# Kernel optimization log

Hardware: AMD Instinct MI355X
Metric: run time of the kernel (lower is better)

Reference implementation:

```python
import jax, jax.numpy as jnp
import numpy as np

B, C = 2048, 512          # batch, channels
CHG = 16                  # coarse grid side (16x16 -> N=256)
FHG = 16                  # fine grid side (16x16 -> F=256)
N = CHG * CHG             # coarse_span.total
F = FHG * FHG             # fine_total
K = 4                     # top4 sample mode
LOG_F = float(np.log(F))


def _ln(x, g, b, eps=1e-5):
    m = jnp.mean(x, axis=-1, keepdims=True)
    v = jnp.var(x, axis=-1, keepdims=True)
    return (x - m) * jax.lax.rsqrt(v + eps) * g + b


def _mlp3(x, w1, b1, w2, b2, w3, b3):
    # linear_stack: Linear+gelu, Linear+gelu, Linear (dropout=0 / eval)
    h = jax.nn.gelu(x @ w1 + b1)
    h = jax.nn.gelu(h @ w2 + b2)
    return h @ w3 + b3


def setup_inputs() -> dict:
    key = jax.random.key(0)
    ks = jax.random.split(key, 10)
    s = 0.02
    return {
        'x': jax.random.normal(ks[0], (B, C), jnp.float32),
        'in_g': jnp.ones((C,), jnp.float32), 'in_b': jnp.zeros((C,), jnp.float32),
        'nop_w': jax.random.normal(ks[1], (C, 1), jnp.float32) * s,
        'nop_b': jnp.zeros((1,), jnp.float32),
        'c_w1': jax.random.normal(ks[2], (C, C), jnp.float32) * s,
        'c_b1': jnp.zeros((C,), jnp.float32),
        'c_w2': jax.random.normal(ks[3], (C, C), jnp.float32) * s,
        'c_b2': jnp.zeros((C,), jnp.float32),
        'c_w3': jax.random.normal(ks[4], (C, N), jnp.float32) * s,
        'c_b3': jnp.zeros((N,), jnp.float32),
        'emb': jax.random.normal(ks[5], (N, C), jnp.float32),
        'emb_g': jnp.ones((C,), jnp.float32), 'emb_b': jnp.zeros((C,), jnp.float32),
        'f_w1': jax.random.normal(ks[6], (2 * C, C), jnp.float32) * s,
        'f_b1': jnp.zeros((C,), jnp.float32),
        'f_w2': jax.random.normal(ks[7], (C, C), jnp.float32) * s,
        'f_b2': jnp.zeros((C,), jnp.float32),
        'f_w3': jax.random.normal(ks[8], (C, F), jnp.float32) * s,
        'f_b3': jnp.zeros((F,), jnp.float32),
    }


def reference(x, in_g, in_b, nop_w, nop_b, c_w1, c_b1, c_w2, c_b2, c_w3, c_b3,
              emb, emb_g, emb_b, f_w1, f_b1, f_w2, f_b2, f_w3, f_b3):
    xn = _ln(x, in_g, in_b)                                  # (B,C)
    no_op = xn @ nop_w + nop_b                               # (B,1)
    coarse = _mlp3(xn, c_w1, c_b1, c_w2, c_b2, c_w3, c_b3)   # (B,N)
    _, idx = jax.lax.top_k(coarse, K)                        # (B,K) int32
    e = _ln(emb[idx], emb_g, emb_b)                          # (B,K,C)
    fin = jnp.concatenate([jnp.broadcast_to(xn[:, None, :], (B, K, C)), e], axis=-1)
    fine = _mlp3(fin, f_w1, f_b1, f_w2, f_b2, f_w3, f_b3)    # (B,K,F)
    # scatter value: coarse[b,i] - log F + fine + log F - lse(fine) = coarse[b,i] + log_softmax(fine)
    vals = jnp.take_along_axis(coarse, idx, axis=1)[:, :, None] + jax.nn.log_softmax(fine, axis=-1)
    dense = jnp.broadcast_to((coarse - LOG_F)[:, :, None], (B, N, F))
    dense = dense.at[jnp.arange(B)[:, None], idx].set(vals)  # top-k indices are distinct
    # view (B, ch0, ch1, fh0, fh1) -> permute (0,1,3,2,4) -> flatten
    xname = dense.reshape(B, CHG, CHG, FHG, FHG).transpose(0, 1, 3, 2, 4).reshape(B, -1)
    return jnp.concatenate([no_op, xname], axis=-1)          # (B, 1 + N*F)
```

## Files before the change

kernel.cpp:

```cpp
#include <hip/hip_runtime.h>
#include <math.h>

#define BATCH 2048
#define CH 512
#define N_COARSE 256
#define F_FINE 256
#define K_TOP 4
#define OUT_STRIDE 65537

typedef unsigned short ushort_t;
typedef __bf16 bf16x8 __attribute__((ext_vector_type(8)));
typedef float f32x4 __attribute__((ext_vector_type(4)));

__device__ __forceinline__ float gelu_tanh(float x) {
    float x3 = x * x * x;
    float t = tanhf(0.7978845608028654f * (x + 0.044715f * x3));
    return 0.5f * x * (1.0f + t);
}

__device__ __forceinline__ ushort_t f2bf(float f) {
    unsigned u = __float_as_uint(f);
    unsigned r = (u + 0x7FFF + ((u >> 16) & 1)) >> 16;
    return (ushort_t)r;
}

__global__ __launch_bounds__(256) void prep_kernel(
    const float* __restrict__ w1, const float* __restrict__ w2, const float* __restrict__ w3,
    ushort_t* __restrict__ t1, ushort_t* __restrict__ t2, ushort_t* __restrict__ t3,
    const float* __restrict__ x, const float* __restrict__ g, const float* __restrict__ b,
    const float* __restrict__ nop_w, const float* __restrict__ nop_b,
    float* __restrict__ xn, ushort_t* __restrict__ xn_bf, float* __restrict__ out)
{
    int blk = blockIdx.x;
    int t = threadIdx.x;
    if (blk < 896) {
        __shared__ float s[32][33];
        const float* W; ushort_t* Wt; int Kd, Nd, gx, gy;
        if (blk < 512)      { W = w1; Wt = t1; Kd = 1024; Nd = 512; gx = blk & 15; gy = blk >> 4; }
        else if (blk < 768) { W = w2; Wt = t2; Kd = 512;  Nd = 512; gx = (blk - 512) & 15; gy = (blk - 512) >> 4; }
        else                { W = w3; Wt = t3; Kd = 512;  Nd = 256; gx = (blk - 768) & 7;  gy = (blk - 768) >> 3; }
        int tx = t & 31, ty = t >> 5;
        int n0 = gx * 32, k0 = gy * 32;
        #pragma unroll
        for (int i = 0; i < 4; ++i) {
            int r = ty + i * 8;
            s[r][tx] = W[(size_t)(k0 + r) * Nd + n0 + tx];
        }
        __syncthreads();
        #pragma unroll
        for (int i = 0; i < 4; ++i) {
            int r = ty + i * 8;
            Wt[(size_t)(n0 + r) * Kd + k0 + tx] = f2bf(s[tx][r]);
        }
    } else {
        int row = blk - 896;
        int lane = t & 63, wave = t >> 6;
        const float* xr = x + (size_t)row * CH;
        float v0 = xr[t], v1 = xr[t + 256];
        float s = v0 + v1, ss = v0 * v0 + v1 * v1;
        #pragma unroll
        for (int off = 32; off; off >>= 1) { s += __shfl_xor(s, off); ss += __shfl_xor(ss, off); }
        __shared__ float red[8];
        if (lane == 0) { red[wave] = s; red[4 + wave] = ss; }
        __syncthreads();
        s = red[0] + red[1] + red[2] + red[3];
        ss = red[4] + red[5] + red[6] + red[7];
        float mean = s * (1.0f / CH);
        float var = ss * (1.0f / CH) - mean * mean;
        float rsq = rsqrtf(var + 1e-5f);
        float xn0 = (v0 - mean) * rsq * g[t] + b[t];
        float xn1 = (v1 - mean) * rsq * g[t + 256] + b[t + 256];
        float* xnr = xn + (size_t)row * CH;
        xnr[t] = xn0; xnr[t + 256] = xn1;
        ushort_t* xbr = xn_bf + (size_t)row * CH;
        xbr[t] = f2bf(xn0); xbr[t + 256] = f2bf(xn1);
        float d = xn0 * nop_w[t] + xn1 * nop_w[t + 256];
        #pragma unroll
        for (int off = 32; off; off >>= 1) d += __shfl_xor(d, off);
        __syncthreads();
        if (lane == 0) red[wave] = d;
        __syncthreads();
        if (t == 0) out[(size_t)row * OUT_STRIDE] = red[0] + red[1] + red[2] + red[3] + nop_b[0];
    }
}

template<bool GELU>
__global__ __launch_bounds__(256) void gemm_kernel(
    const float* __restrict__ A, const float* __restrict__ W,
    const float* __restrict__ bias, float* __restrict__ Cmat, int Nd, int Kd)
{
    __shared__ float As[2][32][68];
    __shared__ float Ws[2][32][36];
    int t = threadIdx.x;
    int tx = t & 7, ty = t >> 3;
    int n0 = blockIdx.x * 32, m0 = blockIdx.y * 64;

    float4 aR[2]; float4 wR;
    float acc[2][4] = {};

    auto loadAB = [&](int k0) {
        #pragma unroll
        for (int i = 0; i < 2; ++i) {
            int c = i * 256 + t;
            aR[i] = *(const float4*)&A[(size_t)(m0 + (c >> 3)) * Kd + k0 + (c & 7) * 4];
        }
        wR = *(const float4*)&W[(size_t)(k0 + (t >> 3)) * Nd + n0 + (t & 7) * 4];
    };
    auto storeAB = [&](int p) {
        #pragma unroll
        for (int i = 0; i < 2; ++i) {
            int c = i * 256 + t, r = c >> 3, kq = (c & 7) * 4;
            As[p][kq + 0][r] = aR[i].x; As[p][kq + 1][r] = aR[i].y;
            As[p][kq + 2][r] = aR[i].z; As[p][kq + 3][r] = aR[i].w;
        }
        *(float4*)&Ws[p][t >> 3][(t & 7) * 4] = wR;
    };

    loadAB(0);
    storeAB(0);
    int steps = Kd >> 5;
    int p = 0;
    for (int s = 0; s < steps; ++s) {
        __syncthreads();
        if (s + 1 < steps) loadAB((s + 1) * 32);
        #pragma unroll
        for (int kk = 0; kk < 32; ++kk) {
            float2 a = *(const float2*)&As[p][kk][ty * 2];
            float4 w = *(const float4*)&Ws[p][kk][tx * 4];
            acc[0][0] += a.x * w.x; acc[0][1] += a.x * w.y; acc[0][2] += a.x * w.z; acc[0][3] += a.x * w.w;
            acc[1][0] += a.y * w.x; acc[1][1] += a.y * w.y; acc[1][2] += a.y * w.z; acc[1][3] += a.y * w.w;
        }
        if (s + 1 < steps) storeAB(p ^ 1);
        p ^= 1;
    }

    #pragma unroll
    for (int i = 0; i < 2; ++i) {
        int gm = m0 + ty * 2 + i;
        int gn0 = n0 + tx * 4;
        float4 o;
        float* po = &o.x;
        #pragma unroll
        for (int j = 0; j < 4; ++j) {
            float v = acc[i][j] + bias[gn0 + j];
            if (GELU) v = gelu_tanh(v);
            po[j] = v;
        }
        *(float4*)&Cmat[(size_t)gm * Nd + gn0] = o;
    }
}

template<int MT, int NT, bool CONCAT, bool GELU, bool OUT_BF16, bool LOGSM>
__global__ __launch_bounds__(256) void mfma_gemm_kernel(
    const ushort_t* __restrict__ A1, const ushort_t* __restrict__ A2, int K1,
    const ushort_t* __restrict__ Wt, const float* __restrict__ bias,
    const float* __restrict__ cvals, void* __restrict__ Cout, int Nd, int Ktot)
{
    constexpr int AI = MT / 64, BI = NT / 64;
    constexpr int FI = MT / 32, FJ = NT / 32;
    __shared__ ushort_t As[2][MT * 32];
    __shared__ ushort_t Bs[2][NT * 32];
    __shared__ float mxs[64][2];
    __shared__ float ses[64][2];
    int t = threadIdx.x;
    int n0 = blockIdx.x * NT, m0 = blockIdx.y * MT;
    int wave = t >> 6, lane = t & 63;
    int wm = (wave & 1) * (MT / 2), wn = (wave >> 1) * (NT / 2);
    int lr = lane & 15, quad = lane >> 4;

    f32x4 acc[FI][FJ] = {};
    float4 aReg[AI], bReg[BI];

    auto loadAB = [&](int k0) {
        #pragma unroll
        for (int i = 0; i < AI; ++i) {
            int c = i * 256 + t, r = c >> 2, q = (c & 3) * 8;
            int gr = m0 + r;
            const ushort_t* ap;
            if (CONCAT) ap = (k0 < K1) ? A1 + (size_t)(gr >> 2) * K1 + k0 + q
                                       : A2 + (size_t)gr * (Ktot - K1) + (k0 - K1) + q;
            else        ap = A1 + (size_t)gr * Ktot + k0 + q;
            aReg[i] = *(const float4*)ap;
        }
        #pragma unroll
        for (int i = 0; i < BI; ++i) {
            int c = i * 256 + t, r = c >> 2, q = (c & 3) * 8;
            bReg[i] = *(const float4*)(Wt + (size_t)(n0 + r) * Ktot + k0 + q);
        }
    };
    auto storeAB = [&](int p) {
        #pragma unroll
        for (int i = 0; i < AI; ++i) { int c = i * 256 + t; *(float4*)&As[p][c * 8] = aReg[i]; }
        #pragma unroll
        for (int i = 0; i < BI; ++i) { int c = i * 256 + t; *(float4*)&Bs[p][c * 8] = bReg[i]; }
    };

    loadAB(0);
    storeAB(0);
    int steps = Ktot >> 5;
    int p = 0;
    for (int s = 0; s < steps; ++s) {
        __syncthreads();
        if (s + 1 < steps) loadAB((s + 1) * 32);
        bf16x8 af[FI], bfr[FJ];
        #pragma unroll
        for (int i = 0; i < FI; ++i)
            af[i] = *(const bf16x8*)&As[p][(wm + i * 16 + lr) * 32 + quad * 8];
        #pragma unroll
        for (int j = 0; j < FJ; ++j)
            bfr[j] = *(const bf16x8*)&Bs[p][(wn + j * 16 + lr) * 32 + quad * 8];
        #pragma unroll
        for (int i = 0; i < FI; ++i)
            #pragma unroll
            for (int j = 0; j < FJ; ++j)
                acc[i][j] = __builtin_amdgcn_mfma_f32_16x16x32_bf16(af[i], bfr[j], acc[i][j], 0, 0, 0);
        if (s + 1 < steps) storeAB(p ^ 1);
        p ^= 1;
    }

    if (LOGSM) {
        float bv[FJ];
        #pragma unroll
        for (int j = 0; j < FJ; ++j) bv[j] = bias[wn + j * 16 + lr];
        int half = wave >> 1;
        float rmx[FI][4];
        #pragma unroll
        for (int i = 0; i < FI; ++i)
            #pragma unroll
            for (int r = 0; r < 4; ++r) {
                float m = -1e30f;
                #pragma unroll
                for (int j = 0; j < FJ; ++j) m = fmaxf(m, acc[i][j][r] + bv[j]);
                #pragma unroll
                for (int mk = 1; mk < 16; mk <<= 1) m = fmaxf(m, __shfl_xor(m, mk));
                if (lr == 0) mxs[wm + i * 16 + quad * 4 + r][half] = m;
            }
        __syncthreads();
        #pragma unroll
        for (int i = 0; i < FI; ++i)
            #pragma unroll
            for (int r = 0; r < 4; ++r) {
                int rl = wm + i * 16 + quad * 4 + r;
                rmx[i][r] = fmaxf(mxs[rl][0], mxs[rl][1]);
            }
        #pragma unroll
        for (int i = 0; i < FI; ++i)
            #pragma unroll
            for (int r = 0; r < 4; ++r) {
                float s = 0.f;
                #pragma unroll
                for (int j = 0; j < FJ; ++j) s += expf(acc[i][j][r] + bv[j] - rmx[i][r]);
                #pragma unroll
                for (int mk = 1; mk < 16; mk <<= 1) s += __shfl_xor(s, mk);
                if (lr == 0) ses[wm + i * 16 + quad * 4 + r][half] = s;
            }
        __syncthreads();
        float* outp = (float*)Cout;
        #pragma unroll
        for (int i = 0; i < FI; ++i)
            #pragma unroll
            for (int r = 0; r < 4; ++r) {
                int rl = wm + i * 16 + quad * 4 + r;
                float se = ses[rl][0] + ses[rl][1];
                float addc = cvals[m0 + rl] - rmx[i][r] - logf(se);
                #pragma unroll
                for (int j = 0; j < FJ; ++j)
                    outp[(size_t)(m0 + rl) * Nd + wn + j * 16 + lr] = acc[i][j][r] + bv[j] + addc;
            }
    } else {
        #pragma unroll
        for (int j = 0; j < FJ; ++j) {
            int col = n0 + wn + j * 16 + lr;
            float bvv = bias[col];
            #pragma unroll
            for (int i = 0; i < FI; ++i) {
                #pragma unroll
                for (int r = 0; r < 4; ++r) {
                    int row = m0 + wm + i * 16 + quad * 4 + r;
                    float val = acc[i][j][r] + bvv;
                    if (GELU) val = gelu_tanh(val);
                    if (OUT_BF16)
                        ((ushort_t*)Cout)[(size_t)row * Nd + col] = f2bf(val);
                    else
                        ((float*)Cout)[(size_t)row * Nd + col] = val;
                }
            }
        }
    }
}

__global__ __launch_bounds__(256) void topk_embln_kernel(
    const float* __restrict__ coarse, const float* __restrict__ emb,
    const float* __restrict__ g, const float* __restrict__ b,
    int* __restrict__ idx, float* __restrict__ cvals, ushort_t* __restrict__ e_bf)
{
    int brow = blockIdx.x;
    int t = threadIdx.x;
    int wave = t >> 6, lane = t & 63;
    __shared__ int sidx[4];

    if (wave == 0) {
        const float* cr = coarse + (size_t)brow * N_COARSE;
        float v[4]; int id[4];
        #pragma unroll
        for (int j = 0; j < 4; ++j) { v[j] = cr[lane + 64 * j]; id[j] = lane + 64 * j; }
        #pragma unroll
        for (int r = 0; r < K_TOP; ++r) {
            float bv = v[0]; int bi = id[0];
            #pragma unroll
            for (int j = 1; j < 4; ++j)
                if (v[j] > bv || (v[j] == bv && id[j] < bi)) { bv = v[j]; bi = id[j]; }
            #pragma unroll
            for (int off = 32; off; off >>= 1) {
                float ov = __shfl_xor(bv, off); int oi = __shfl_xor(bi, off);
                if (ov > bv || (ov == bv && oi < bi)) { bv = ov; bi = oi; }
            }
            if ((bi & 63) == lane) v[bi >> 6] = -INFINITY;
            if (lane == 0) {
                sidx[r] = bi;
                idx[brow * K_TOP + r] = bi;
                cvals[brow * K_TOP + r] = bv;
            }
        }
    }
    __syncthreads();

    int n = sidx[wave];
    const float* er = emb + (size_t)n * CH + lane * 8;
    float4 u0 = *(const float4*)er;
    float4 u1 = *(const float4*)(er + 4);
    float s  = u0.x + u0.y + u0.z + u0.w + u1.x + u1.y + u1.z + u1.w;
    float ss = u0.x * u0.x + u0.y * u0.y + u0.z * u0.z + u0.w * u0.w
             + u1.x * u1.x + u1.y * u1.y + u1.z * u1.z + u1.w * u1.w;
    #pragma unroll
    for (int off = 32; off; off >>= 1) { s += __shfl_xor(s, off); ss += __shfl_xor(ss, off); }
    float mean = s * (1.0f / CH);
    float var = ss * (1.0f / CH) - mean * mean;
    float rsq = rsqrtf(var + 1e-5f);
    float4 g0 = *(const float4*)(g + lane * 8), g1 = *(const float4*)(g + lane * 8 + 4);
    float4 b0 = *(const float4*)(b + lane * 8), b1 = *(const float4*)(b + lane * 8 + 4);
    uint4 pk;
    pk.x = (unsigned)f2bf((u0.x - mean) * rsq * g0.x + b0.x) |
           ((unsigned)f2bf((u0.y - mean) * rsq * g0.y + b0.y) << 16);
    pk.y = (unsigned)f2bf((u0.z - mean) * rsq * g0.z + b0.z) |
           ((unsigned)f2bf((u0.w - mean) * rsq * g0.w + b0.w) << 16);
    pk.z = (unsigned)f2bf((u1.x - mean) * rsq * g1.x + b1.x) |
           ((unsigned)f2bf((u1.y - mean) * rsq * g1.y + b1.y) << 16);
    pk.w = (unsigned)f2bf((u1.z - mean) * rsq * g1.z + b1.z) |
           ((unsigned)f2bf((u1.w - mean) * rsq * g1.w + b1.w) << 16);
    *(uint4*)(e_bf + (size_t)(brow * K_TOP + wave) * CH + lane * 8) = pk;
}

__global__ __launch_bounds__(256) void scatter_kernel(
    const float* __restrict__ coarse, const float* __restrict__ fine,
    const int* __restrict__ idx, float* __restrict__ out)
{
    const float LOG_F = 5.545177444479562f;
    int b = blockIdx.y;
    __shared__ int sidx[4];
    if (threadIdx.x < 4) sidx[threadIdx.x] = idx[b * 4 + threadIdx.x];
    __syncthreads();
    int i0 = sidx[0], i1 = sidx[1], i2 = sidx[2], i3 = sidx[3];
    size_t rowb = (size_t)b * OUT_STRIDE + 1;
    #pragma unroll
    for (int q = 0; q < 4; ++q) {
        int o = blockIdx.x * 4096 + q * 1024 + threadIdx.x * 4;
        int c0 = o >> 12, f0 = (o >> 8) & 15, c1 = (o >> 4) & 15, f1 = o & 15;
        int n = c0 * 16 + c1;
        int f = f0 * 16 + f1;
        int k = -1;
        if (n == i0) k = 0; else if (n == i1) k = 1; else if (n == i2) k = 2; else if (n == i3) k = 3;
        float r0, r1, r2, r3;
        if (k >= 0) {
            float4 u = *(const float4*)(fine + ((size_t)(b * 4 + k)) * F_FINE + f);
            r0 = u.x; r1 = u.y; r2 = u.z; r3 = u.w;
        } else {
            float base = coarse[(size_t)b * N_COARSE + n] - LOG_F;
            r0 = r1 = r2 = r3 = base;
        }
        float* p = out + rowb + o;
        __builtin_nontemporal_store(r0, p + 0);
        __builtin_nontemporal_store(r1, p + 1);
        __builtin_nontemporal_store(r2, p + 2);
        __builtin_nontemporal_store(r3, p + 3);
    }
}

extern "C" void kernel_launch(void* const* d_in, const int* in_sizes, int n_in,
                              void* d_out, int out_size, void* d_ws, size_t ws_size,
                              hipStream_t stream) {
    const float* x     = (const float*)d_in[0];
    const float* in_g  = (const float*)d_in[1];
    const float* in_b  = (const float*)d_in[2];
    const float* nop_w = (const float*)d_in[3];
    const float* nop_b = (const float*)d_in[4];
    const float* c_w1  = (const float*)d_in[5];
    const float* c_b1  = (const float*)d_in[6];
    const float* c_w2  = (const float*)d_in[7];
    const float* c_b2  = (const float*)d_in[8];
    const float* c_w3  = (const float*)d_in[9];
    const float* c_b3  = (const float*)d_in[10];
    const float* emb   = (const float*)d_in[11];
    const float* emb_g = (const float*)d_in[12];
    const float* emb_b = (const float*)d_in[13];
    const float* f_w1  = (const float*)d_in[14];
    const float* f_b1  = (const float*)d_in[15];
    const float* f_w2  = (const float*)d_in[16];
    const float* f_b2  = (const float*)d_in[17];
    const float* f_w3  = (const float*)d_in[18];
    const float* f_b3  = (const float*)d_in[19];

    float* ws = (float*)d_ws;
    float* xn      = ws;
    float* h1      = xn + 1048576;
    float* h2      = h1 + 1048576;
    float* coarse  = h2 + 1048576;
    float* fine    = coarse + 524288;
    ushort_t* xn_bf  = (ushort_t*)(fine + 2097152);
    ushort_t* e_bf   = xn_bf + 1048576;
    ushort_t* fh1_bf = e_bf + 4194304;
    ushort_t* fh2_bf = fh1_bf + 4194304;
    ushort_t* wt1    = fh2_bf + 4194304;
    ushort_t* wt2    = wt1 + 524288;
    ushort_t* wt3    = wt2 + 262144;
    int*   idxb   = (int*)(wt3 + 131072);
    float* cvals  = (float*)(idxb + 8192);

    float* out = (float*)d_out;

    prep_kernel<<<896 + BATCH, 256, 0, stream>>>(
        f_w1, f_w2, f_w3, wt1, wt2, wt3,
        x, in_g, in_b, nop_w, nop_b, xn, xn_bf, out);
    gemm_kernel<true><<<dim3(16, 32), 256, 0, stream>>>(xn, c_w1, c_b1, h1, 512, 512);
    gemm_kernel<true><<<dim3(16, 32), 256, 0, stream>>>(h1, c_w2, c_b2, h2, 512, 512);
    gemm_kernel<false><<<dim3(8, 32), 256, 0, stream>>>(h2, c_w3, c_b3, coarse, 256, 512);
    topk_embln_kernel<<<BATCH, 256, 0, stream>>>(coarse, emb, emb_g, emb_b, idxb, cvals, e_bf);
    mfma_gemm_kernel<64, 128, true, true, true, false><<<dim3(4, 128), 256, 0, stream>>>(
        xn_bf, e_bf, 512, wt1, f_b1, nullptr, fh1_bf, 512, 1024);
    mfma_gemm_kernel<64, 128, false, true, true, false><<<dim3(4, 128), 256, 0, stream>>>(
        fh1_bf, nullptr, 0, wt2, f_b2, nullptr, fh2_bf, 512, 512);
    mfma_gemm_kernel<64, 256, false, false, false, true><<<dim3(1, 128), 256, 0, stream>>>(
        fh2_bf, nullptr, 0, wt3, f_b3, cvals, fine, 256, 512);
    scatter_kernel<<<dim3(16, BATCH), 256, 0, stream>>>(coarse, fine, idxb, out);
}
```

Before: 777.4 us.

## Run coarse MLP on bf16 MFMA with split hi/lo bf16 compensation

Replaces the three fp32 SIMT GEMMs of the coarse MLP with the bf16 MFMA GEMM. Each operand is split into high and low bf16 parts, and three MFMA products (hi*hi, lo*hi, hi*lo) are accumulated over a K extent of 1536 to approximate fp32 accuracy. This keeps top-k selection stable. The prep kernel now also transposes and splits the coarse weights and writes xn as a hi/lo pair. The gemm templates are reorganized around MODE/OUTM parameters. The aim is to move the coarse path off slow fp32 FMA onto matrix cores, at the cost of three times the MMA work and slightly different rounding, which could flip near-tie top-k choices.

```diff
diff --git a/kernel.cpp b/kernel.cpp
--- a/kernel.cpp
+++ b/kernel.cpp
@@ -23,22 +23,30 @@
     unsigned r = (u + 0x7FFF + ((u >> 16) & 1)) >> 16;
     return (ushort_t)r;
 }
+__device__ __forceinline__ float bf2f(ushort_t h) {
+    return __uint_as_float(((unsigned)h) << 16);
+}
 
 __global__ __launch_bounds__(256) void prep_kernel(
-    const float* __restrict__ w1, const float* __restrict__ w2, const float* __restrict__ w3,
-    ushort_t* __restrict__ t1, ushort_t* __restrict__ t2, ushort_t* __restrict__ t3,
+    const float* __restrict__ f_w1, const float* __restrict__ f_w2, const float* __restrict__ f_w3,
+    ushort_t* __restrict__ wt1, ushort_t* __restrict__ wt2, ushort_t* __restrict__ wt3,
+    const float* __restrict__ c_w1, const float* __restrict__ c_w2, const float* __restrict__ c_w3,
+    ushort_t* __restrict__ cwt1, ushort_t* __restrict__ cwt2, ushort_t* __restrict__ cwt3,
     const float* __restrict__ x, const float* __restrict__ g, const float* __restrict__ b,
     const float* __restrict__ nop_w, const float* __restrict__ nop_b,
-    float* __restrict__ xn, ushort_t* __restrict__ xn_bf, float* __restrict__ out)
+    ushort_t* __restrict__ xnsp, float* __restrict__ out)
 {
+    __shared__ float s[32][33];
     int blk = blockIdx.x;
     int t = threadIdx.x;
-    if (blk < 896) {
-        __shared__ float s[32][33];
-        const float* W; ushort_t* Wt; int Kd, Nd, gx, gy;
-        if (blk < 512)      { W = w1; Wt = t1; Kd = 1024; Nd = 512; gx = blk & 15; gy = blk >> 4; }
-        else if (blk < 768) { W = w2; Wt = t2; Kd = 512;  Nd = 512; gx = (blk - 512) & 15; gy = (blk - 512) >> 4; }
-        else                { W = w3; Wt = t3; Kd = 512;  Nd = 256; gx = (blk - 768) & 7;  gy = (blk - 768) >> 3; }
+    if (blk < 1536) {
+        const float* W; ushort_t* Wt; int Kd, Nd, gx, gy; bool split;
+        if (blk < 512)       { W=f_w1; Wt=wt1; Kd=1024; Nd=512; gx=blk&15; gy=blk>>4; split=false; }
+        else if (blk < 768)  { int u=blk-512;  W=f_w2; Wt=wt2; Kd=512; Nd=512; gx=u&15; gy=u>>4; split=false; }
+        else if (blk < 896)  { int u=blk-768;  W=f_w3; Wt=wt3; Kd=512; Nd=256; gx=u&7;  gy=u>>3; split=false; }
+        else if (blk < 1152) { int u=blk-896;  W=c_w1; Wt=cwt1; Kd=512; Nd=512; gx=u&15; gy=u>>4; split=true; }
+        else if (blk < 1408) { int u=blk-1152; W=c_w2; Wt=cwt2; Kd=512; Nd=512; gx=u&15; gy=u>>4; split=true; }
+        else                 { int u=blk-1408; W=c_w3; Wt=cwt3; Kd=512; Nd=256; gx=u&7;  gy=u>>3; split=true; }
         int tx = t & 31, ty = t >> 5;
         int n0 = gx * 32, k0 = gy * 32;
         #pragma unroll
@@ -47,33 +55,45 @@
             s[r][tx] = W[(size_t)(k0 + r) * Nd + n0 + tx];
         }
         __syncthreads();
-        #pragma unroll
-        for (int i = 0; i < 4; ++i) {
-            int r = ty + i * 8;
-            Wt[(size_t)(n0 + r) * Kd + k0 + tx] = f2bf(s[tx][r]);
+        if (!split) {
+            #pragma unroll
+            for (int i = 0; i < 4; ++i) {
+                int r = ty + i * 8;
+                Wt[(size_t)(n0 + r) * Kd + k0 + tx] = f2bf(s[tx][r]);
+            }
+        } else {
+            #pragma unroll
+            for (int i = 0; i < 4; ++i) {
+                int r = ty + i * 8;
+                float v = s[tx][r];
+                ushort_t h = f2bf(v);
+                Wt[(size_t)(n0 + r) * 1024 + k0 + tx] = h;
+                Wt[(size_t)(n0 + r) * 1024 + 512 + k0 + tx] = f2bf(v - bf2f(h));
+            }
         }
     } else {
-        int row = blk - 896;
+        float* red = &s[0][0];
+        int row = blk - 1536;
         int lane = t & 63, wave = t >> 6;
         const float* xr = x + (size_t)row * CH;
         float v0 = xr[t], v1 = xr[t + 256];
-        float s = v0 + v1, ss = v0 * v0 + v1 * v1;
-        #pragma unroll
-        for (int off = 32; off; off >>= 1) { s += __shfl_xor(s, off); ss += __shfl_xor(ss, off); }
-        __shared__ float red[8];
-        if (lane == 0) { red[wave] = s; red[4 + wave] = ss; }
-        __syncthreads();
-        s = red[0] + red[1] + red[2] + red[3];
+        float sm = v0 + v1, ss = v0 * v0 + v1 * v1;
+        #pragma unroll
+        for (int off = 32; off; off >>= 1) { sm += __shfl_xor(sm, off); ss += __shfl_xor(ss, off); }
+        if (lane == 0) { red[wave] = sm; red[4 + wave] = ss; }
+        __syncthreads();
+        sm = red[0] + red[1] + red[2] + red[3];
         ss = red[4] + red[5] + red[6] + red[7];
-        float mean = s * (1.0f / CH);
+        float mean = sm * (1.0f / CH);
         float var = ss * (1.0f / CH) - mean * mean;
         float rsq = rsqrtf(var + 1e-5f);
         float xn0 = (v0 - mean) * rsq * g[t] + b[t];
         float xn1 = (v1 - mean) * rsq * g[t + 256] + b[t + 256];
-        float* xnr = xn + (size_t)row * CH;
-        xnr[t] = xn0; xnr[t + 256] = xn1;
-        ushort_t* xbr = xn_bf + (size_t)row * CH;
-        xbr[t] = f2bf(xn0); xbr[t + 256] = f2bf(xn1);
+        ushort_t* xr2 = xnsp + (size_t)row * 1024;
+        ushort_t h0 = f2bf(xn0), h1v = f2bf(xn1);
+        xr2[t] = h0; xr2[t + 256] = h1v;
+        xr2[512 + t] = f2bf(xn0 - bf2f(h0));
+        xr2[512 + t + 256] = f2bf(xn1 - bf2f(h1v));
         float d = xn0 * nop_w[t] + xn1 * nop_w[t + 256];
         #pragma unroll
         for (int off = 32; off; off >>= 1) d += __shfl_xor(d, off);
@@ -84,75 +104,9 @@
     }
 }
 
-template<bool GELU>
-__global__ __launch_bounds__(256) void gemm_kernel(
-    const float* __restrict__ A, const float* __restrict__ W,
-    const float* __restrict__ bias, float* __restrict__ Cmat, int Nd, int Kd)
-{
-    __shared__ float As[2][32][68];
-    __shared__ float Ws[2][32][36];
-    int t = threadIdx.x;
-    int tx = t & 7, ty = t >> 3;
-    int n0 = blockIdx.x * 32, m0 = blockIdx.y * 64;
-
-    float4 aR[2]; float4 wR;
-    float acc[2][4] = {};
-
-    auto loadAB = [&](int k0) {
-        #pragma unroll
-        for (int i = 0; i < 2; ++i) {
-            int c = i * 256 + t;
-            aR[i] = *(const float4*)&A[(size_t)(m0 + (c >> 3)) * Kd + k0 + (c & 7) * 4];
-        }
-        wR = *(const float4*)&W[(size_t)(k0 + (t >> 3)) * Nd + n0 + (t & 7) * 4];
-    };
-    auto storeAB = [&](int p) {
-        #pragma unroll
-        for (int i = 0; i < 2; ++i) {
-            int c = i * 256 + t, r = c >> 3, kq = (c & 7) * 4;
-            As[p][kq + 0][r] = aR[i].x; As[p][kq + 1][r] = aR[i].y;
-            As[p][kq + 2][r] = aR[i].z; As[p][kq + 3][r] = aR[i].w;
-        }
-        *(float4*)&Ws[p][t >> 3][(t & 7) * 4] = wR;
-    };
-
-    loadAB(0);
-    storeAB(0);
-    int steps = Kd >> 5;
-    int p = 0;
-    for (int s = 0; s < steps; ++s) {
-        __syncthreads();
-        if (s + 1 < steps) loadAB((s + 1) * 32);
-        #pragma unroll
-        for (int kk = 0; kk < 32; ++kk) {
-            float2 a = *(const float2*)&As[p][kk][ty * 2];
-            float4 w = *(const float4*)&Ws[p][kk][tx * 4];
-            acc[0][0] += a.x * w.x; acc[0][1] += a.x * w.y; acc[0][2] += a.x * w.z; acc[0][3] += a.x * w.w;
-            acc[1][0] += a.y * w.x; acc[1][1] += a.y * w.y; acc[1][2] += a.y * w.z; acc[1][3] += a.y * w.w;
-        }
-        if (s + 1 < steps) storeAB(p ^ 1);
-        p ^= 1;
-    }
-
-    #pragma unroll
-    for (int i = 0; i < 2; ++i) {
-        int gm = m0 + ty * 2 + i;
-        int gn0 = n0 + tx * 4;
-        float4 o;
-        float* po = &o.x;
-        #pragma unroll
-        for (int j = 0; j < 4; ++j) {
-            float v = acc[i][j] + bias[gn0 + j];
-            if (GELU) v = gelu_tanh(v);
-            po[j] = v;
-        }
-        *(float4*)&Cmat[(size_t)gm * Nd + gn0] = o;
-    }
-}
-
-template<int MT, int NT, bool CONCAT, bool GELU, bool OUT_BF16, bool LOGSM>
+template<int MODE, int MT, int NT, int OUTM>
 __global__ __launch_bounds__(256) void mfma_gemm_kernel(
-    const ushort_t* __restrict__ A1, const ushort_t* __restrict__ A2, int K1,
+    const ushort_t* __restrict__ A1, const ushort_t* __restrict__ A2,
     const ushort_t* __restrict__ Wt, const float* __restrict__ bias,
     const float* __restrict__ cvals, void* __restrict__ Cout, int Nd, int Ktot)
 {
@@ -160,8 +114,8 @@
     constexpr int FI = MT / 32, FJ = NT / 32;
     __shared__ ushort_t As[2][MT * 32];
     __shared__ ushort_t Bs[2][NT * 32];
-    __shared__ float mxs[64][2];
-    __shared__ float ses[64][2];
+    __shared__ float mxs[64 * 2];
+    __shared__ float ses[64 * 2];
     int t = threadIdx.x;
     int n0 = blockIdx.x * NT, m0 = blockIdx.y * MT;
     int wave = t >> 6, lane = t & 63;
@@ -172,20 +126,24 @@
     float4 aReg[AI], bReg[BI];
 
     auto loadAB = [&](int k0) {
+        int aoff = (MODE == 2) ? ((k0 >= 1024) ? k0 - 512 : (k0 & 511)) : k0;
+        int woff = (MODE == 2) ? ((k0 >= 1024) ? k0 - 1024 : k0) : k0;
         #pragma unroll
         for (int i = 0; i < AI; ++i) {
             int c = i * 256 + t, r = c >> 2, q = (c & 3) * 8;
             int gr = m0 + r;
             const ushort_t* ap;
-            if (CONCAT) ap = (k0 < K1) ? A1 + (size_t)(gr >> 2) * K1 + k0 + q
-                                       : A2 + (size_t)gr * (Ktot - K1) + (k0 - K1) + q;
-            else        ap = A1 + (size_t)gr * Ktot + k0 + q;
+            if (MODE == 1)      ap = (k0 < 512) ? A1 + (size_t)(gr >> 2) * 1024 + k0 + q
+                                                : A2 + (size_t)gr * 512 + (k0 - 512) + q;
+            else if (MODE == 2) ap = A1 + (size_t)gr * 1024 + aoff + q;
+            else                ap = A1 + (size_t)gr * Ktot + k0 + q;
             aReg[i] = *(const float4*)ap;
         }
         #pragma unroll
         for (int i = 0; i < BI; ++i) {
             int c = i * 256 + t, r = c >> 2, q = (c & 3) * 8;
-            bReg[i] = *(const float4*)(Wt + (size_t)(n0 + r) * Ktot + k0 + q);
+            size_t wstride = (MODE == 2) ? 1024 : (size_t)Ktot;
+            bReg[i] = *(const float4*)(Wt + (size_t)(n0 + r) * wstride + woff + q);
         }
     };
     auto storeAB = [&](int p) {
@@ -218,7 +176,7 @@
         p ^= 1;
     }
 
-    if (LOGSM) {
+    if (OUTM == 3) {
         float bv[FJ];
         #pragma unroll
         for (int j = 0; j < FJ; ++j) bv[j] = bias[wn + j * 16 + lr];
@@ -233,7 +191,7 @@
                 for (int j = 0; j < FJ; ++j) m = fmaxf(m, acc[i][j][r] + bv[j]);
                 #pragma unroll
                 for (int mk = 1; mk < 16; mk <<= 1) m = fmaxf(m, __shfl_xor(m, mk));
-                if (lr == 0) mxs[wm + i * 16 + quad * 4 + r][half] = m;
+                if (lr == 0) mxs[(wm + i * 16 + quad * 4 + r) * 2 + half] = m;
             }
         __syncthreads();
         #pragma unroll
@@ -241,18 +199,18 @@
             #pragma unroll
             for (int r = 0; r < 4; ++r) {
                 int rl = wm + i * 16 + quad * 4 + r;
-                rmx[i][r] = fmaxf(mxs[rl][0], mxs[rl][1]);
+                rmx[i][r] = fmaxf(mxs[rl * 2], mxs[rl * 2 + 1]);
             }
         #pragma unroll
         for (int i = 0; i < FI; ++i)
             #pragma unroll
             for (int r = 0; r < 4; ++r) {
-                float s = 0.f;
-                #pragma unroll
-                for (int j = 0; j < FJ; ++j) s += expf(acc[i][j][r] + bv[j] - rmx[i][r]);
-                #pragma unroll
-                for (int mk = 1; mk < 16; mk <<= 1) s += __shfl_xor(s, mk);
-                if (lr == 0) ses[wm + i * 16 + quad * 4 + r][half] = s;
+                float sv = 0.f;
+                #pragma unroll
+                for (int j = 0; j < FJ; ++j) sv += expf(acc[i][j][r] + bv[j] - rmx[i][r]);
+                #pragma unroll
+                for (int mk = 1; mk < 16; mk <<= 1) sv += __shfl_xor(sv, mk);
+                if (lr == 0) ses[(wm + i * 16 + quad * 4 + r) * 2 + half] = sv;
             }
         __syncthreads();
         float* outp = (float*)Cout;
@@ -261,7 +219,7 @@
             #pragma unroll
             for (int r = 0; r < 4; ++r) {
                 int rl = wm + i * 16 + quad * 4 + r;
-                float se = ses[rl][0] + ses[rl][1];
+                float se = ses[rl * 2] + ses[rl * 2 + 1];
                 float addc = cvals[m0 + rl] - rmx[i][r] - logf(se);
                 #pragma unroll
                 for (int j = 0; j < FJ; ++j)
@@ -278,11 +236,16 @@
                 for (int r = 0; r < 4; ++r) {
                     int row = m0 + wm + i * 16 + quad * 4 + r;
                     float val = acc[i][j][r] + bvv;
-                    if (GELU) val = gelu_tanh(val);
-                    if (OUT_BF16)
-                        ((ushort_t*)Cout)[(size_t)row * Nd + col] = f2bf(val);
-                    else
+                    if (OUTM == 0) {
+                        ((ushort_t*)Cout)[(size_t)row * Nd + col] = f2bf(gelu_tanh(val));
+                    } else if (OUTM == 1) {
+                        float gv = gelu_tanh(val);
+                        ushort_t h = f2bf(gv);
+                        ((ushort_t*)Cout)[(size_t)row * 1024 + col] = h;
+                        ((ushort_t*)Cout)[(size_t)row * 1024 + 512 + col] = f2bf(gv - bf2f(h));
+                    } else {
                         ((float*)Cout)[(size_t)row * Nd + col] = val;
+                    }
                 }
             }
         }
@@ -411,35 +374,41 @@
     const float* f_b3  = (const float*)d_in[19];
 
     float* ws = (float*)d_ws;
-    float* xn      = ws;
-    float* h1      = xn + 1048576;
-    float* h2      = h1 + 1048576;
-    float* coarse  = h2 + 1048576;
+    float* coarse  = ws;
     float* fine    = coarse + 524288;
-    ushort_t* xn_bf  = (ushort_t*)(fine + 2097152);
-    ushort_t* e_bf   = xn_bf + 1048576;
+    ushort_t* xnsp   = (ushort_t*)(fine + 2097152);
+    ushort_t* h1sp   = xnsp + 2097152;
+    ushort_t* h2sp   = h1sp + 2097152;
+    ushort_t* e_bf   = h2sp + 2097152;
     ushort_t* fh1_bf = e_bf + 4194304;
     ushort_t* fh2_bf = fh1_bf + 4194304;
     ushort_t* wt1    = fh2_bf + 4194304;
     ushort_t* wt2    = wt1 + 524288;
     ushort_t* wt3    = wt2 + 262144;
-    int*   idxb   = (int*)(wt3 + 131072);
+    ushort_t* cwt1   = wt3 + 131072;
+    ushort_t* cwt2   = cwt1 + 524288;
+    ushort_t* cwt3   = cwt2 + 524288;
+    int*   idxb   = (int*)(cwt3 + 262144);
     float* cvals  = (float*)(idxb + 8192);
 
     float* out = (float*)d_out;
 
-    prep_kernel<<<896 + BATCH, 256, 0, stream>>>(
+    prep_kernel<<<3584, 256, 0, stream>>>(
         f_w1, f_w2, f_w3, wt1, wt2, wt3,
-        x, in_g, in_b, nop_w, nop_b, xn, xn_bf, out);
-    gemm_kernel<true><<<dim3(16, 32), 256, 0, stream>>>(xn, c_w1, c_b1, h1, 512, 512);
-    gemm_kernel<true><<<dim3(16, 32), 256, 0, stream>>>(h1, c_w2, c_b2, h2, 512, 512);
-    gemm_kernel<false><<<dim3(8, 32), 256, 0, stream>>>(h2, c_w3, c_b3, coarse, 256, 512);
+        c_w1, c_w2, c_w3, cwt1, cwt2, cwt3,
+        x, in_g, in_b, nop_w, nop_b, xnsp, out);
+    mfma_gemm_kernel<2, 64, 64, 1><<<dim3(8, 32), 256, 0, stream>>>(
+        xnsp, nullptr, cwt1, c_b1, nullptr, h1sp, 512, 1536);
+    mfma_gemm_kernel<2, 64, 64, 1><<<dim3(8, 32), 256, 0, stream>>>(
+        h1sp, nullptr, cwt2, c_b2, nullptr, h2sp, 512, 1536);
+    mfma_gemm_kernel<2, 64, 64, 2><<<dim3(4, 32), 256, 0, stream>>>(
+        h2sp, nullptr, cwt3, c_b3, nullptr, coarse, 256, 1536);
     topk_embln_kernel<<<BATCH, 256, 0, stream>>>(coarse, emb, emb_g, emb_b, idxb, cvals, e_bf);
-    mfma_gemm_kernel<64, 128, true, true, true, false><<<dim3(4, 128), 256, 0, stream>>>(
-        xn_bf, e_bf, 512, wt1, f_b1, nullptr, fh1_bf, 512, 1024);
-    mfma_gemm_kernel<64, 128, false, true, true, false><<<dim3(4, 128), 256, 0, stream>>>(
-        fh1_bf, nullptr, 0, wt2, f_b2, nullptr, fh2_bf, 512, 512);
-    mfma_gemm_kernel<64, 256, false, false, false, true><<<dim3(1, 128), 256, 0, stream>>>(
-        fh2_bf, nullptr, 0, wt3, f_b3, cvals, fine, 256, 512);
+    mfma_gemm_kernel<1, 64, 128, 0><<<dim3(4, 128), 256, 0, stream>>>(
+        xnsp, e_bf, wt1, f_b1, nullptr, fh1_bf, 512, 1024);
+    mfma_gemm_kernel<0, 64, 128, 0><<<dim3(4, 128), 256, 0, stream>>>(
+        fh1_bf, nullptr, wt2, f_b2, nullptr, fh2_bf, 512, 512);
+    mfma_gemm_kernel<0, 64, 256, 3><<<dim3(1, 128), 256, 0, stream>>>(
+        fh2_bf, nullptr, wt3, f_b3, cvals, fine, 256, 512);
     scatter_kernel<<<dim3(16, BATCH), 256, 0, stream>>>(coarse, fine, idxb, out);
 }
```

Measured after the change: 760.2 us. 2.2% less time.
